# Kernel optimization log

Measured on AMD Instinct MI355X. Metric: run time of the kernel, lower is better.

Reference implementation:

```python
import jax, jax.numpy as jnp
import numpy as np

D_MODEL = 1024
D_STATE = 16
EXPAND = 2
D_CONV = 4
D_INNER = EXPAND * D_MODEL
BATCH = 1
SEQLEN = 2048


def setup_inputs() -> dict:
    key = jax.random.key(0)
    ks = jax.random.split(key, 8)
    s = 0.02
    x = jax.random.normal(ks[0], (BATCH, SEQLEN, D_MODEL), jnp.float32)
    W_in = jax.random.normal(ks[1], (2 * D_INNER, D_MODEL), jnp.float32) * s
    conv_w = jax.random.normal(ks[2], (D_INNER, 1, D_CONV), jnp.float32) * s
    conv_b = jnp.zeros((D_INNER,), jnp.float32)
    # A_log init as in module: log(arange(1, d_state+1)) tiled over d_inner
    A_log = jnp.log(jnp.tile(jnp.arange(1, D_STATE + 1, dtype=jnp.float32), (D_INNER, 1)))
    D_param = jnp.ones((D_INNER,), jnp.float32)
    W_x = jax.random.normal(ks[3], (2 * D_STATE, D_INNER), jnp.float32) * s
    W_dt = jax.random.normal(ks[4], (D_INNER, D_INNER), jnp.float32) * s
    b_dt = jnp.zeros((D_INNER,), jnp.float32)
    W_out = jax.random.normal(ks[5], (D_MODEL, D_INNER), jnp.float32) * s
    return {"x": x, "W_in": W_in, "conv_w": conv_w, "conv_b": conv_b,
            "A_log": A_log, "D_param": D_param, "W_x": W_x,
            "W_dt": W_dt, "b_dt": b_dt, "W_out": W_out}


def reference(x, W_in, conv_w, conv_b, A_log, D_param, W_x, W_dt, b_dt, W_out):
    B_, L, _ = x.shape
    xz = jnp.einsum('bld,ed->ble', x, W_in)          # [B,L,2*d_inner]
    x_inner, z = jnp.split(xz, 2, axis=-1)
    # causal depthwise conv1d (pad left d_conv-1 == torch pad-both + slice[:L])
    xc = jax.lax.conv_general_dilated(
        jnp.swapaxes(x_inner, 1, 2), conv_w, (1,), [(D_CONV - 1, 0)],
        feature_group_count=D_INNER,
        dimension_numbers=('NCH', 'OIH', 'NCH')) + conv_b[None, :, None]
    x_ssm = jnp.swapaxes(jax.nn.silu(xc), 1, 2)       # [B,L,d_inner]
    dt = jax.nn.softplus(jnp.einsum('ble,fe->blf', x_ssm, W_dt) + b_dt)
    x_dbl = jnp.einsum('ble,se->bls', x_ssm, W_x)     # [B,L,2*d_state]
    B_mat, C_mat = jnp.split(x_dbl, 2, axis=-1)       # each [B,L,d_state]
    A = -jnp.exp(A_log)                               # [d_inner,d_state]
    dA = jnp.exp(dt[..., None] * A)                   # [B,L,d_inner,d_state]
    dBx = B_mat[:, :, None, :] * dt[..., None] * x_ssm[..., None]

    def step(h, inp):
        dA_t, dBx_t, C_t = inp
        h = dA_t * h + dBx_t                          # [B,d_inner,d_state]
        y_t = jnp.einsum('bds,bs->bd', h, C_t)
        return h, y_t

    h0 = jnp.zeros((B_, D_INNER, D_STATE), x.dtype)
    _, ys = jax.lax.scan(step, h0, (jnp.swapaxes(dA, 0, 1),
                                    jnp.swapaxes(dBx, 0, 1),
                                    jnp.swapaxes(C_mat, 0, 1)))
    y = jnp.swapaxes(ys, 0, 1) + D_param * x_ssm      # [B,L,d_inner]
    y = y * jax.nn.silu(z)
    out = jnp.einsum('ble,de->bld', y, W_out)
    return out + x
```

## Files before the change

### kernel.cpp

```cpp
#include <hip/hip_runtime.h>

#define L_SEQ 2048
#define DMODEL 1024
#define DINNER 2048
#define NCHUNK 128
#define TCHUNK 16

typedef __attribute__((ext_vector_type(8))) short bf16x8;
typedef __attribute__((ext_vector_type(4))) float f32x4;

__device__ __forceinline__ float bf2f(unsigned short u) {
  return __uint_as_float(((unsigned)u) << 16);
}
__device__ __forceinline__ unsigned short f2bf(float f) {
  unsigned u = __float_as_uint(f);
  return (unsigned short)((u + 0x7FFFu + ((u >> 16) & 1u)) >> 16);
}
__device__ __forceinline__ void gload_lds16(const void* g, void* l) {
  __builtin_amdgcn_global_load_lds(
      (const __attribute__((address_space(1))) void*)g,
      (__attribute__((address_space(3))) void*)l, 16, 0, 0);
}

__global__ void cvt_f32_bf16(const float4* __restrict__ in, ushort4* __restrict__ out, int n4) {
  int i = blockIdx.x * blockDim.x + threadIdx.x;
  if (i >= n4) return;
  float4 v = in[i];
  ushort4 o;
  o.x = f2bf(v.x); o.y = f2bf(v.y); o.z = f2bf(v.z); o.w = f2bf(v.w);
  out[i] = o;
}

__global__ void zero_bf16(ushort4* __restrict__ out, int n4) {
  int i = blockIdx.x * blockDim.x + threadIdx.x;
  if (i >= n4) return;
  out[i] = ushort4{0, 0, 0, 0};
}

template <int EPI>
__global__ __launch_bounds__(256) void gemm_bt2(
    const unsigned short* __restrict__ A, const unsigned short* __restrict__ B,
    int M, int N, int K, int nx, int ksplit,
    float* __restrict__ outf, unsigned short* __restrict__ outb,
    const float* __restrict__ aux) {
  __shared__ __align__(16) unsigned short As[2 * 128 * 32];
  __shared__ __align__(16) unsigned short Bs[2 * 128 * 32];
  const int tid = threadIdx.x;
  const int lane = tid & 63;
  const int wave = tid >> 6;
  const int wm = wave >> 1, wn = wave & 1;

  const int nwg = gridDim.x;
  const int wg = blockIdx.x;
  const int swz = (wg & 7) * (nwg >> 3) + (wg >> 3);
  const int tiles = nwg / ksplit;
  const int ks = swz / tiles;
  const int t = swz - ks * tiles;
  const int bx = t % nx, by = t / nx;
  const int bm = by * 128, bn = bx * 128;
  const int Ks = K / ksplit;
  const int kbeg = ks * Ks, kend = ks * Ks + Ks;

  const int srow = tid >> 2, sc4 = tid & 3;
  const unsigned short* Ag = A + (size_t)(bm + srow) * K + sc4 * 8;
  const unsigned short* Bg = B + (size_t)(bn + srow) * K + sc4 * 8;
  unsigned short* AsW = &As[srow * 32 + sc4 * 8];
  unsigned short* BsW = &Bs[srow * 32 + sc4 * 8];

  auto STAGE = [&](int buf, int k0) {
    gload_lds16(Ag + k0, AsW + buf * 4096);
    gload_lds16(Ag + (size_t)64 * K + k0, AsW + buf * 4096 + 64 * 32);
    gload_lds16(Bg + k0, BsW + buf * 4096);
    gload_lds16(Bg + (size_t)64 * K + k0, BsW + buf * 4096 + 64 * 32);
  };

  f32x4 acc[4][4] = {};

  STAGE(0, kbeg);
  __syncthreads();

  const int kz = (lane >> 4) * 8;
  const int r16 = lane & 15;

  for (int k0 = kbeg; k0 < kend; k0 += 32) {
    int cur = ((k0 - kbeg) >> 5) & 1;
    if (k0 + 32 < kend) STAGE(cur ^ 1, k0 + 32);

    bf16x8 a[4], b[4];
#pragma unroll
    for (int i = 0; i < 4; ++i)
      a[i] = *(const bf16x8*)&As[cur * 4096 + (wm * 64 + i * 16 + r16) * 32 + kz];
#pragma unroll
    for (int j = 0; j < 4; ++j)
      b[j] = *(const bf16x8*)&Bs[cur * 4096 + (wn * 64 + j * 16 + r16) * 32 + kz];
#pragma unroll
    for (int i = 0; i < 4; ++i)
#pragma unroll
      for (int j = 0; j < 4; ++j)
        acc[i][j] = __builtin_amdgcn_mfma_f32_16x16x32_bf16(a[i], b[j], acc[i][j], 0, 0, 0);

    __syncthreads();
  }

  const int rq = lane >> 4;
#pragma unroll
  for (int i = 0; i < 4; ++i)
#pragma unroll
    for (int j = 0; j < 4; ++j)
#pragma unroll
      for (int r = 0; r < 4; ++r) {
        int row = bm + wm * 64 + i * 16 + rq * 4 + r;
        int col = bn + wn * 64 + j * 16 + r16;
        float v = acc[i][j][r];
        if (EPI == 0) {
          outb[(size_t)row * N + col] = f2bf(v);
        } else if (EPI == 3) {
          if (col < 2048) {
            float tt = v + aux[col];
            float sp = (tt > 15.f) ? tt : log1pf(__expf(tt));
            outb[(size_t)row * 2048 + col] = f2bf(sp);
          } else if (col < 2080) {
            outf[(size_t)row * 32 + (col - 2048)] = v;
          }
        } else {
          outf[(size_t)ks * M * N + (size_t)row * N + col] = v;
        }
      }
}

__global__ void reduce_addx(const float4* __restrict__ p, const float4* __restrict__ x,
                            float4* __restrict__ out, int n4) {
  int i = blockIdx.x * 256 + threadIdx.x;
  if (i >= n4) return;
  float4 a = p[i], b = p[n4 + i], c = x[i];
  float4 o;
  o.x = a.x + b.x + c.x; o.y = a.y + b.y + c.y;
  o.z = a.z + b.z + c.z; o.w = a.w + b.w + c.w;
  out[i] = o;
}

__global__ __launch_bounds__(256) void conv_silu8(
    const unsigned short* __restrict__ xz,
    const float* __restrict__ cw, const float* __restrict__ cb,
    unsigned short* __restrict__ x_ssm, unsigned short* __restrict__ sz_out) {
  int idx = blockIdx.x * 256 + threadIdx.x;
  int l = idx >> 8, c0 = (idx & 255) * 8;
  float acc[8];
  float4 b0 = *(const float4*)(cb + c0);
  float4 b1 = *(const float4*)(cb + c0 + 4);
  acc[0] = b0.x; acc[1] = b0.y; acc[2] = b0.z; acc[3] = b0.w;
  acc[4] = b1.x; acc[5] = b1.y; acc[6] = b1.z; acc[7] = b1.w;
  float4 w[8];
#pragma unroll
  for (int j = 0; j < 8; ++j) w[j] = *(const float4*)(cw + (c0 + j) * 4);
#pragma unroll
  for (int k = 0; k < 4; ++k) {
    int lt = l - 3 + k;
    if (lt >= 0) {
      bf16x8 v = *(const bf16x8*)(xz + (size_t)lt * 4096 + c0);
      const float* wk = (const float*)w;
#pragma unroll
      for (int j = 0; j < 8; ++j)
        acc[j] = fmaf(bf2f((unsigned short)v[j]), wk[j * 4 + k], acc[j]);
    }
  }
  bf16x8 zr = *(const bf16x8*)(xz + (size_t)l * 4096 + 2048 + c0);
  bf16x8 ox, oz;
#pragma unroll
  for (int j = 0; j < 8; ++j) {
    float a = acc[j];
    ox[j] = (short)f2bf(a / (1.f + __expf(-a)));
    float zv = bf2f((unsigned short)zr[j]);
    oz[j] = (short)f2bf(zv / (1.f + __expf(-zv)));
  }
  *(bf16x8*)(x_ssm + (size_t)idx * 8) = ox;
  *(bf16x8*)(sz_out + (size_t)idx * 8) = oz;
}

__global__ __launch_bounds__(256) void scan_passA(
    const unsigned short* __restrict__ dtb, const unsigned short* __restrict__ x_ssm,
    const float* __restrict__ x_dbl, const float* __restrict__ A_log,
    float* __restrict__ Pout, float* __restrict__ Hout) {
  int tid = threadIdx.x;
  int c = blockIdx.x & (NCHUNK - 1), db = blockIdx.x >> 7;
  int d = db * 256 + tid;
  int t0 = c * TCHUNK;
  float Av[16];
  const float4* al4 = (const float4*)(A_log + d * 16);
#pragma unroll
  for (int q = 0; q < 4; ++q) {
    float4 a = al4[q];
    Av[q * 4 + 0] = -__expf(a.x); Av[q * 4 + 1] = -__expf(a.y);
    Av[q * 4 + 2] = -__expf(a.z); Av[q * 4 + 3] = -__expf(a.w);
  }
  float h[16];
#pragma unroll
  for (int s = 0; s < 16; ++s) h[s] = 0.f;
  float sum_dt = 0.f;
#pragma unroll 2
  for (int i = 0; i < TCHUNK; ++i) {
    int t = t0 + i;
    float dtv = bf2f(dtb[(size_t)t * 2048 + d]);
    float xv = bf2f(x_ssm[(size_t)t * 2048 + d]);
    float dtx = dtv * xv;
    sum_dt += dtv;
    const float* B = x_dbl + t * 32;
#pragma unroll
    for (int s = 0; s < 16; ++s) {
      float dA = __expf(dtv * Av[s]);
      h[s] = fmaf(dA, h[s], B[s] * dtx);
    }
  }
  float* Ho = Hout + (size_t)c * 32768 + d * 16;
  float* Po = Pout + (size_t)c * 32768 + d * 16;
#pragma unroll
  for (int s = 0; s < 16; ++s) Ho[s] = h[s];
#pragma unroll
  for (int s = 0; s < 16; ++s) Po[s] = __expf(sum_dt * Av[s]);
}

__global__ __launch_bounds__(256) void scan_passB(
    float* __restrict__ P, const float* __restrict__ Hloc) {
  int i = blockIdx.x * 256 + threadIdx.x;
  float h = 0.f;
  for (int c = 0; c < NCHUNK; ++c) {
    size_t o = (size_t)c * 32768 + i;
    float p = P[o];
    float hl = Hloc[o];
    P[o] = h;
    h = fmaf(p, h, hl);
  }
}

__global__ __launch_bounds__(256) void scan_passC(
    const unsigned short* __restrict__ dtb, const unsigned short* __restrict__ x_ssm,
    const float* __restrict__ x_dbl, const float* __restrict__ A_log,
    const float* __restrict__ D_param, const unsigned short* __restrict__ silu_z,
    const float* __restrict__ Hinit, unsigned short* __restrict__ y_out) {
  int tid = threadIdx.x;
  int c = blockIdx.x & (NCHUNK - 1), db = blockIdx.x >> 7;
  int d = db * 256 + tid;
  int t0 = c * TCHUNK;
  float Av[16];
  const float4* al4 = (const float4*)(A_log + d * 16);
#pragma unroll
  for (int q = 0; q < 4; ++q) {
    float4 a = al4[q];
    Av[q * 4 + 0] = -__expf(a.x); Av[q * 4 + 1] = -__expf(a.y);
    Av[q * 4 + 2] = -__expf(a.z); Av[q * 4 + 3] = -__expf(a.w);
  }
  float Dp = D_param[d];
  float h[16];
  const float4* hi4 = (const float4*)(Hinit + (size_t)c * 32768 + d * 16);
#pragma unroll
  for (int q = 0; q < 4; ++q) {
    float4 v = hi4[q];
    h[q * 4 + 0] = v.x; h[q * 4 + 1] = v.y; h[q * 4 + 2] = v.z; h[q * 4 + 3] = v.w;
  }
#pragma unroll 2
  for (int i = 0; i < TCHUNK; ++i) {
    int t = t0 + i;
    float dtv = bf2f(dtb[(size_t)t * 2048 + d]);
    float xv = bf2f(x_ssm[(size_t)t * 2048 + d]);
    float dtx = dtv * xv;
    const float* B = x_dbl + t * 32;
    const float* C = x_dbl + t * 32 + 16;
    float y = 0.f;
#pragma unroll
    for (int s = 0; s < 16; ++s) {
      float dA = __expf(dtv * Av[s]);
      h[s] = fmaf(dA, h[s], B[s] * dtx);
      y = fmaf(h[s], C[s], y);
    }
    float szv = bf2f(silu_z[(size_t)t * 2048 + d]);
    y_out[(size_t)t * 2048 + d] = f2bf((y + Dp * xv) * szv);
  }
}

extern "C" void kernel_launch(void* const* d_in, const int* in_sizes, int n_in,
                              void* d_out, int out_size, void* d_ws, size_t ws_size,
                              hipStream_t stream) {
  const float* x      = (const float*)d_in[0];
  const float* W_in   = (const float*)d_in[1];
  const float* conv_w = (const float*)d_in[2];
  const float* conv_b = (const float*)d_in[3];
  const float* A_log  = (const float*)d_in[4];
  const float* D_par  = (const float*)d_in[5];
  const float* W_x    = (const float*)d_in[6];
  const float* W_dt   = (const float*)d_in[7];
  const float* b_dt   = (const float*)d_in[8];
  const float* W_out  = (const float*)d_in[9];
  float* out = (float*)d_out;

  char* ws = (char*)d_ws;
  unsigned short* xbf    = (unsigned short*)(ws + 0);
  unsigned short* Winbf  = (unsigned short*)(ws + ((size_t)4 << 20));
  unsigned short* Wcomb  = (unsigned short*)(ws + ((size_t)12 << 20));
  unsigned short* Woutbf = (unsigned short*)(ws + ((size_t)21 << 20));
  unsigned short* xz     = (unsigned short*)(ws + ((size_t)25 << 20));
  unsigned short* xssm   = (unsigned short*)(ws + ((size_t)41 << 20));
  unsigned short* siluz  = (unsigned short*)(ws + ((size_t)49 << 20));
  unsigned short* dtb    = (unsigned short*)(ws + ((size_t)57 << 20));
  float* xdbl            = (float*)(ws + ((size_t)65 << 20));
  unsigned short* yfin   = (unsigned short*)(ws + ((size_t)66 << 20));
  float* Pbuf            = (float*)(ws + ((size_t)25 << 20));
  float* Hloc            = (float*)(ws + ((size_t)4 << 20));
  float* part            = (float*)(ws + ((size_t)41 << 20));

  cvt_f32_bf16<<<2048, 256, 0, stream>>>((const float4*)x, (ushort4*)xbf, (L_SEQ * DMODEL) / 4);
  cvt_f32_bf16<<<4096, 256, 0, stream>>>((const float4*)W_in, (ushort4*)Winbf, (2 * DINNER * DMODEL) / 4);
  cvt_f32_bf16<<<4096, 256, 0, stream>>>((const float4*)W_dt, (ushort4*)Wcomb, (DINNER * DINNER) / 4);
  cvt_f32_bf16<<<64, 256, 0, stream>>>((const float4*)W_x, (ushort4*)(Wcomb + (size_t)2048 * 2048),
                                       (32 * DINNER) / 4);
  zero_bf16<<<192, 256, 0, stream>>>((ushort4*)(Wcomb + (size_t)2080 * 2048), (96 * DINNER) / 4);
  cvt_f32_bf16<<<2048, 256, 0, stream>>>((const float4*)W_out, (ushort4*)Woutbf, (DMODEL * DINNER) / 4);

  gemm_bt2<0><<<512, 256, 0, stream>>>(xbf, Winbf, L_SEQ, 4096, DMODEL, 32, 1,
                                       nullptr, xz, nullptr);

  conv_silu8<<<2048, 256, 0, stream>>>(xz, conv_w, conv_b, xssm, siluz);

  gemm_bt2<3><<<272, 256, 0, stream>>>(xssm, Wcomb, L_SEQ, 2176, DINNER, 17, 1,
                                       xdbl, dtb, b_dt);

  scan_passA<<<NCHUNK * (DINNER / 256), 256, 0, stream>>>(dtb, xssm, xdbl, A_log, Pbuf, Hloc);
  scan_passB<<<(DINNER * 16) / 256, 256, 0, stream>>>(Pbuf, Hloc);
  scan_passC<<<NCHUNK * (DINNER / 256), 256, 0, stream>>>(dtb, xssm, xdbl, A_log, D_par, siluz,
                                                          Pbuf, yfin);

  gemm_bt2<4><<<256, 256, 0, stream>>>(yfin, Woutbf, L_SEQ, DMODEL, DINNER, 8, 2,
                                       part, nullptr, nullptr);
  reduce_addx<<<(L_SEQ * DMODEL / 4 + 255) / 256, 256, 0, stream>>>(
      (const float4*)part, (const float4*)x, (float4*)out, L_SEQ * DMODEL / 4);
}
```

Baseline: 321.8 us.

## Triple-buffer GEMM LDS staging with vmcnt waits and XOR-swizzled layout

Moves the bf16 GEMM from double to triple-buffered LDS staging. Each iteration waits on the outstanding global-to-LDS loads with s_waitcnt vmcnt and a single barrier instead of two __syncthreads, which keeps two tiles in flight. It also XOR-swizzles the 16-byte column chunk on both the global source address and the LDS read offset to reduce LDS bank conflicts. The cost is 50% more LDS per block, which may reduce occupancy, plus hand-tuned wait counts that must match the number of loads per stage.

```diff
diff --git a/kernel.cpp b/kernel.cpp
--- a/kernel.cpp
+++ b/kernel.cpp
@@ -38,13 +38,13 @@
 }
 
 template <int EPI>
-__global__ __launch_bounds__(256) void gemm_bt2(
+__global__ __launch_bounds__(256) void gemm_bt3(
     const unsigned short* __restrict__ A, const unsigned short* __restrict__ B,
     int M, int N, int K, int nx, int ksplit,
     float* __restrict__ outf, unsigned short* __restrict__ outb,
     const float* __restrict__ aux) {
-  __shared__ __align__(16) unsigned short As[2 * 128 * 32];
-  __shared__ __align__(16) unsigned short Bs[2 * 128 * 32];
+  __shared__ __align__(16) unsigned short As[3 * 128 * 32];
+  __shared__ __align__(16) unsigned short Bs[3 * 128 * 32];
   const int tid = threadIdx.x;
   const int lane = tid & 63;
   const int wave = tid >> 6;
@@ -52,18 +52,20 @@
 
   const int nwg = gridDim.x;
   const int wg = blockIdx.x;
-  const int swz = (wg & 7) * (nwg >> 3) + (wg >> 3);
+  const int swzb = (wg & 7) * (nwg >> 3) + (wg >> 3);
   const int tiles = nwg / ksplit;
-  const int ks = swz / tiles;
-  const int t = swz - ks * tiles;
+  const int ks = swzb / tiles;
+  const int t = swzb - ks * tiles;
   const int bx = t % nx, by = t / nx;
   const int bm = by * 128, bn = bx * 128;
   const int Ks = K / ksplit;
-  const int kbeg = ks * Ks, kend = ks * Ks + Ks;
+  const int kbeg = ks * Ks;
+  const int nk = Ks >> 5;
 
   const int srow = tid >> 2, sc4 = tid & 3;
-  const unsigned short* Ag = A + (size_t)(bm + srow) * K + sc4 * 8;
-  const unsigned short* Bg = B + (size_t)(bn + srow) * K + sc4 * 8;
+  const int scp = sc4 ^ ((srow >> 1) & 3);
+  const unsigned short* Ag = A + (size_t)(bm + srow) * K + scp * 8;
+  const unsigned short* Bg = B + (size_t)(bn + srow) * K + scp * 8;
   unsigned short* AsW = &As[srow * 32 + sc4 * 8];
   unsigned short* BsW = &Bs[srow * 32 + sc4 * 8];
 
@@ -76,30 +78,41 @@
 
   f32x4 acc[4][4] = {};
 
+  const int g = lane >> 4;
+  const int r16 = lane & 15;
+  const int sw = (g ^ ((r16 >> 1) & 3)) * 8;
+
   STAGE(0, kbeg);
-  __syncthreads();
-
-  const int kz = (lane >> 4) * 8;
-  const int r16 = lane & 15;
-
-  for (int k0 = kbeg; k0 < kend; k0 += 32) {
-    int cur = ((k0 - kbeg) >> 5) & 1;
-    if (k0 + 32 < kend) STAGE(cur ^ 1, k0 + 32);
+  STAGE(1, kbeg + 32);
+  int cur = 0, stg = 2;
+
+  for (int i = 0; i < nk; ++i) {
+    if (i < nk - 1) {
+      asm volatile("s_waitcnt vmcnt(4)" ::: "memory");
+    } else {
+      asm volatile("s_waitcnt vmcnt(0)" ::: "memory");
+    }
+    __builtin_amdgcn_s_barrier();
+    asm volatile("" ::: "memory");
+    if (i + 2 < nk) {
+      STAGE(stg, kbeg + (i + 2) * 32);
+      stg = (stg == 2) ? 0 : stg + 1;
+    }
 
     bf16x8 a[4], b[4];
 #pragma unroll
-    for (int i = 0; i < 4; ++i)
-      a[i] = *(const bf16x8*)&As[cur * 4096 + (wm * 64 + i * 16 + r16) * 32 + kz];
+    for (int ii = 0; ii < 4; ++ii)
+      a[ii] = *(const bf16x8*)&As[cur * 4096 + (wm * 64 + ii * 16 + r16) * 32 + sw];
 #pragma unroll
     for (int j = 0; j < 4; ++j)
-      b[j] = *(const bf16x8*)&Bs[cur * 4096 + (wn * 64 + j * 16 + r16) * 32 + kz];
-#pragma unroll
-    for (int i = 0; i < 4; ++i)
+      b[j] = *(const bf16x8*)&Bs[cur * 4096 + (wn * 64 + j * 16 + r16) * 32 + sw];
+#pragma unroll
+    for (int ii = 0; ii < 4; ++ii)
 #pragma unroll
       for (int j = 0; j < 4; ++j)
-        acc[i][j] = __builtin_amdgcn_mfma_f32_16x16x32_bf16(a[i], b[j], acc[i][j], 0, 0, 0);
-
-    __syncthreads();
+        acc[ii][j] = __builtin_amdgcn_mfma_f32_16x16x32_bf16(a[ii], b[j], acc[ii][j], 0, 0, 0);
+
+    cur = (cur == 2) ? 0 : cur + 1;
   }
 
   const int rq = lane >> 4;
@@ -315,12 +328,12 @@
   zero_bf16<<<192, 256, 0, stream>>>((ushort4*)(Wcomb + (size_t)2080 * 2048), (96 * DINNER) / 4);
   cvt_f32_bf16<<<2048, 256, 0, stream>>>((const float4*)W_out, (ushort4*)Woutbf, (DMODEL * DINNER) / 4);
 
-  gemm_bt2<0><<<512, 256, 0, stream>>>(xbf, Winbf, L_SEQ, 4096, DMODEL, 32, 1,
+  gemm_bt3<0><<<512, 256, 0, stream>>>(xbf, Winbf, L_SEQ, 4096, DMODEL, 32, 1,
                                        nullptr, xz, nullptr);
 
   conv_silu8<<<2048, 256, 0, stream>>>(xz, conv_w, conv_b, xssm, siluz);
 
-  gemm_bt2<3><<<272, 256, 0, stream>>>(xssm, Wcomb, L_SEQ, 2176, DINNER, 17, 1,
+  gemm_bt3<3><<<272, 256, 0, stream>>>(xssm, Wcomb, L_SEQ, 2176, DINNER, 17, 1,
                                        xdbl, dtb, b_dt);
 
   scan_passA<<<NCHUNK * (DINNER / 256), 256, 0, stream>>>(dtb, xssm, xdbl, A_log, Pbuf, Hloc);
@@ -328,7 +341,7 @@
   scan_passC<<<NCHUNK * (DINNER / 256), 256, 0, stream>>>(dtb, xssm, xdbl, A_log, D_par, siluz,
                                                           Pbuf, yfin);
 
-  gemm_bt2<4><<<256, 256, 0, stream>>>(yfin, Woutbf, L_SEQ, DMODEL, DINNER, 8, 2,
+  gemm_bt3<4><<<256, 256, 0, stream>>>(yfin, Woutbf, L_SEQ, DMODEL, DINNER, 8, 2,
                                        part, nullptr, nullptr);
   reduce_addx<<<(L_SEQ * DMODEL / 4 + 255) / 256, 256, 0, stream>>>(
       (const float4*)part, (const float4*)x, (float4*)out, L_SEQ * DMODEL / 4);
```

New measurement: 320.0 us. No clear change (-0.6%).
